# Kernel optimization log

Measured on AMD Instinct MI355X. Metric: run time of the kernel, lower is better.

## Reference

```python
import jax, jax.numpy as jnp
import numpy as np

E, C, M, H, O = 8, 1024, 2048, 8192, 2048  # experts, capacity, model_dim, hidden, output_dim


def setup_inputs() -> dict:
    key = jax.random.key(0)
    k1, k2, k3, k4, k5 = jax.random.split(key, 5)
    s1 = 1.0 / np.sqrt(M)
    s2 = 1.0 / np.sqrt(H)
    return {
        "x": jax.random.normal(k1, (E, C, M), dtype=jnp.float32),
        "fc1_w": jax.random.normal(k2, (E, H, M), dtype=jnp.float32) * s1,
        "fc1_b": jax.random.normal(k3, (E, H), dtype=jnp.float32) * s1,
        "fc2_w": jax.random.normal(k4, (E, H, O), dtype=jnp.float32) * s2,
        "fc2_b": jax.random.normal(k5, (E, O), dtype=jnp.float32) * s2,
    }


def reference(x, fc1_w, fc1_b, fc2_w, fc2_b):
    # grouped GEMM: per-expert FC1 + bias + ReLU + FC2 + bias
    # x: [E, C, M], fc1_w: [E, H, M], fc2_w: [E, H, O]
    y = jnp.einsum('ecm,ehm->ech', x, fc1_w) + fc1_b[:, None, :]   # [E, C, H]
    y = jax.nn.relu(y)
    y = jnp.einsum('ech,eho->eco', y, fc2_w) + fc2_b[:, None, :]   # [E, C, O]
    return y
```

## Files before the change

### kernel.cpp

```cpp
#include <hip/hip_runtime.h>
#include <hip/hip_bf16.h>
#include <stddef.h>

constexpr int E_ = 8;
constexpr int C_ = 1024;
constexpr int M_ = 2048;
constexpr int H_ = 8192;
constexpr int O_ = 2048;

typedef __bf16 bf16;
typedef __bf16 bf16x4 __attribute__((ext_vector_type(4)));
typedef __bf16 bf16x8 __attribute__((ext_vector_type(8)));
typedef float  f32x4  __attribute__((ext_vector_type(4)));

#define GLOAD16(src, dst)                                                        \
    __builtin_amdgcn_global_load_lds(                                            \
        (const __attribute__((address_space(1))) void*)(src),                    \
        (__attribute__((address_space(3))) void*)(dst), 16, 0, 0)

#define BARRIER()  __builtin_amdgcn_s_barrier()
#define LGKM0()    do { asm volatile("s_waitcnt lgkmcnt(0)" ::: "memory");       \
                        __builtin_amdgcn_sched_barrier(0); } while (0)
#define VMCNT(n)   asm volatile("s_waitcnt vmcnt(" #n ")" ::: "memory")

__global__ __launch_bounds__(256)
void cvt_f32_bf16(const float* __restrict__ in, bf16* __restrict__ out, size_t n)
{
    size_t i = ((size_t)blockIdx.x * blockDim.x + threadIdx.x) * 16;
    const size_t stride = (size_t)gridDim.x * blockDim.x * 16;
    for (; i < n; i += stride) {
        f32x4 v0 = *(const f32x4*)(in + i);
        f32x4 v1 = *(const f32x4*)(in + i + 4);
        f32x4 v2 = *(const f32x4*)(in + i + 8);
        f32x4 v3 = *(const f32x4*)(in + i + 12);
        bf16x8 o0, o1;
#pragma unroll
        for (int j = 0; j < 4; ++j) {
            o0[j] = (bf16)v0[j]; o0[j + 4] = (bf16)v1[j];
            o1[j] = (bf16)v2[j]; o1[j + 4] = (bf16)v3[j];
        }
        *(bf16x8*)(out + i)     = o0;
        *(bf16x8*)(out + i + 8) = o1;
    }
}

__global__ __launch_bounds__(256)
void transpose_w2(const float* __restrict__ W2, bf16* __restrict__ W2t, int e0)
{
    const int e  = e0 + blockIdx.z;
    const int oo = blockIdx.x;
    const int ho = blockIdx.y;
    const int tid = threadIdx.x;

    __shared__ bf16 t[64][72];

    const float* src = W2 + (size_t)e * H_ * O_ + (size_t)(ho * 64) * O_ + oo * 64;
#pragma unroll
    for (int p = 0; p < 4; ++p) {
        const int h  = p * 16 + (tid >> 4);
        const int o4 = (tid & 15) * 4;
        f32x4 v = *(const f32x4*)(src + (size_t)h * O_ + o4);
#pragma unroll
        for (int q = 0; q < 4; ++q) t[o4 + q][h] = (bf16)v[q];
    }
    __syncthreads();

    bf16* dst = W2t + (size_t)blockIdx.z * O_ * H_ + (size_t)(oo * 64) * H_ + ho * 64;
#pragma unroll
    for (int p2 = 0; p2 < 2; ++p2) {
        const int o  = p2 * 32 + (tid >> 3);
        const int h8 = (tid & 7) * 8;
        bf16x8 v = *(const bf16x8*)(&t[o][h8]);
        *(bf16x8*)(dst + (size_t)o * H_ + h8) = v;
    }
}

template<int KDIM, bool RELU_BF16>
__global__ __launch_bounds__(512, 2)
void gemm256(const bf16* __restrict__ A, const bf16* __restrict__ B,
             const float* __restrict__ bias, void* __restrict__ OutP,
             int nBM, int nBN)
{
    extern __shared__ char smem[];
    constexpr int K2  = KDIM * 2;
    constexpr int NIT = KDIM / 128;

    const int tid  = threadIdx.x;
    const int lane = tid & 63;
    const int wid  = tid >> 6;
    const int wr = wid >> 2, wc = wid & 3;
    const int fr = lane & 15, fq = lane >> 4;

    const int nwg = gridDim.x;
    const int cpx = nwg >> 3;
    const int b0  = blockIdx.x;
    const int wg  = (b0 & 7) * cpx + (b0 >> 3);
    const int per_e = nBM * nBN;
    const int e  = wg / per_e;
    const int rr = wg - e * per_e;
    const int bn = rr / nBM;
    const int bm = rr - bn * nBM;
    const int MROWS = nBM * 256;
    const int NROWS = nBN * 256;

    const char* Apan = (const char*)(A + (size_t)e * MROWS * KDIM + (size_t)bm * 256 * KDIM);
    const char* Bpan = (const char*)(B + (size_t)e * NROWS * KDIM + (size_t)bn * 256 * KDIM);

    const int r0  = tid >> 3;
    const int wsw = ((tid & 7) << 4) ^ ((r0 & 7) << 4);

    auto stageA = [&](int gk, int comp) {
        char* lds = smem + (gk & 1) * 65536 + comp * 16384 + tid * 16;
        const char* src = Apan + (size_t)((comp << 7) + r0) * K2 + (size_t)gk * 128 + wsw;
        GLOAD16(src, lds);
        GLOAD16(src + (size_t)64 * K2, lds + 8192);
    };
    auto stageB = [&](int gk, int comp2) {
        char* lds = smem + (gk & 1) * 65536 + 32768 + comp2 * 16384 + tid * 16;
        const char* src = Bpan + (size_t)((comp2 << 7) + r0) * K2 + (size_t)gk * 128 + wsw;
        GLOAD16(src, lds);
        GLOAD16(src + (size_t)64 * K2, lds + 8192);
    };

    const int frq = fr & 7;
    const int cA0 = ((fq    ) ^ frq) << 4;
    const int cA1 = ((4 | fq) ^ frq) << 4;
    const int aoff = wr * 16384 + fr * 128;
    const int boff = 32768 + (wc >> 1) * 16384 + (wc & 1) * 8192 + fr * 128;

    bf16x8 av[4][2];
    bf16x8 bv[4][2];
    f32x4 acc[8][4];
#pragma unroll
    for (int m = 0; m < 8; ++m)
#pragma unroll
        for (int n = 0; n < 4; ++n) acc[m][n] = (f32x4){0.f, 0.f, 0.f, 0.f};

    auto loadA = [&](const char* base, int mh) {
#pragma unroll
        for (int mm = 0; mm < 4; ++mm) {
            const char* p = base + aoff + (mh * 4 + mm) * 2048;
            av[mm][0] = *(const bf16x8*)(p + cA0);
            av[mm][1] = *(const bf16x8*)(p + cA1);
        }
    };
    auto loadB = [&](const char* base, int nh) {
#pragma unroll
        for (int nn = 0; nn < 2; ++nn) {
            const char* p = base + boff + (nh * 2 + nn) * 2048;
            bv[nh * 2 + nn][0] = *(const bf16x8*)(p + cA0);
            bv[nh * 2 + nn][1] = *(const bf16x8*)(p + cA1);
        }
    };
    auto mmaq = [&](int mh, int nh) {
        __builtin_amdgcn_s_setprio(1);
#pragma unroll
        for (int mm = 0; mm < 4; ++mm)
#pragma unroll
            for (int nn = 0; nn < 2; ++nn) {
                const int m = mh * 4 + mm, n = nh * 2 + nn;
                acc[m][n] = __builtin_amdgcn_mfma_f32_16x16x32_bf16(av[mm][0], bv[n][0], acc[m][n], 0, 0, 0);
                acc[m][n] = __builtin_amdgcn_mfma_f32_16x16x32_bf16(av[mm][1], bv[n][1], acc[m][n], 0, 0, 0);
            }
        __builtin_amdgcn_s_setprio(0);
    };

    stageB(0, 0); stageB(0, 1); stageA(0, 0); stageA(0, 1);
    stageB(1, 0); stageB(1, 1);
    VMCNT(4);
    BARRIER();

    for (int t = 0; t < NIT; ++t) {
        const bool nl = (t + 1 < NIT);
        const char* d0b = smem;
        const char* d1b = smem + 65536;
        const int ga = 2 * t + 1;
        const int gb = 2 * t + 2;
        const int gc = 2 * t + 3;

        loadB(d0b, 0); loadA(d0b, 0);
        stageA(ga, 0);
        BARRIER(); LGKM0();
        mmaq(0, 0);
        BARRIER();

        loadB(d0b, 1);
        stageA(ga, 1);
        BARRIER(); LGKM0();
        mmaq(0, 1);
        BARRIER();

        loadA(d0b, 1);
        if (nl) stageB(gb, 0);
        BARRIER(); LGKM0();
        mmaq(1, 1);
        BARRIER();

        if (nl) stageB(gb, 1);
        BARRIER(); LGKM0();
        mmaq(1, 0);
        if (nl) { VMCNT(4); } else { VMCNT(0); }
        BARRIER();

        loadB(d1b, 0); loadA(d1b, 0);
        if (nl) stageA(gb, 0);
        BARRIER(); LGKM0();
        mmaq(0, 0);
        BARRIER();

        loadB(d1b, 1);
        if (nl) stageA(gb, 1);
        BARRIER(); LGKM0();
        mmaq(0, 1);
        BARRIER();

        loadA(d1b, 1);
        if (nl) stageB(gc, 0);
        BARRIER(); LGKM0();
        mmaq(1, 1);
        BARRIER();

        if (nl) stageB(gc, 1);
        BARRIER(); LGKM0();
        mmaq(1, 0);
        if (nl) {
            VMCNT(4);
            BARRIER();
        }
    }

    const int gr0 = bm * 256 + wr * 128;
    const int gc0 = bn * 256 + wc * 64;
    if constexpr (RELU_BF16) {
        bf16* Out = (bf16*)OutP;
#pragma unroll
        for (int n = 0; n < 4; ++n) {
            const int col = gc0 + n * 16 + fr;
            const float bb = bias[(size_t)e * NROWS + col];
#pragma unroll
            for (int m = 0; m < 8; ++m)
#pragma unroll
                for (int j = 0; j < 4; ++j) {
                    float v = acc[m][n][j] + bb;
                    v = v > 0.f ? v : 0.f;
                    const int row = gr0 + m * 16 + fq * 4 + j;
                    Out[((size_t)e * MROWS + row) * NROWS + col] = (bf16)v;
                }
        }
    } else {
        float* Out = (float*)OutP;
#pragma unroll
        for (int n = 0; n < 4; ++n) {
            const int col = gc0 + n * 16 + fr;
            const float bb = bias[(size_t)e * NROWS + col];
#pragma unroll
            for (int m = 0; m < 8; ++m)
#pragma unroll
                for (int j = 0; j < 4; ++j) {
                    const int row = gr0 + m * 16 + fq * 4 + j;
                    Out[((size_t)e * MROWS + row) * NROWS + col] = acc[m][n][j] + bb;
                }
        }
    }
}

template<int KDIM, bool RELU_BF16>
__global__ __launch_bounds__(1024, 1)
void gemm256w16(const bf16* __restrict__ A, const bf16* __restrict__ B,
                const float* __restrict__ bias, void* __restrict__ OutP,
                int nBM, int nBN)
{
    extern __shared__ char smem[];
    constexpr int K2  = KDIM * 2;
    constexpr int NIT = KDIM / 128;

    const int tid  = threadIdx.x;
    const int lane = tid & 63;
    const int wid  = tid >> 6;
    const int wr = wid >> 2, wc = wid & 3;
    const int fr = lane & 15, fq = lane >> 4;

    const int nwg = gridDim.x;
    const int cpx = nwg >> 3;
    const int b0  = blockIdx.x;
    const int wg  = (b0 & 7) * cpx + (b0 >> 3);
    const int per_e = nBM * nBN;
    const int e  = wg / per_e;
    const int rr = wg - e * per_e;
    const int bn = rr / nBM;
    const int bm = rr - bn * nBM;
    const int MROWS = nBM * 256;
    const int NROWS = nBN * 256;

    const char* Apan = (const char*)(A + (size_t)e * MROWS * KDIM + (size_t)bm * 256 * KDIM);
    const char* Bpan = (const char*)(B + (size_t)e * NROWS * KDIM + (size_t)bn * 256 * KDIM);

    const int r0  = tid >> 3;
    const int wsw = ((tid & 7) << 4) ^ ((r0 & 7) << 4);

    auto stageA = [&](int gk, int comp) {
        char* lds = smem + (gk & 1) * 65536 + comp * 16384 + tid * 16;
        const char* src = Apan + (size_t)((comp << 7) + r0) * K2 + (size_t)gk * 128 + wsw;
        GLOAD16(src, lds);
    };
    auto stageB = [&](int gk, int comp2) {
        char* lds = smem + (gk & 1) * 65536 + 32768 + comp2 * 16384 + tid * 16;
        const char* src = Bpan + (size_t)((comp2 << 7) + r0) * K2 + (size_t)gk * 128 + wsw;
        GLOAD16(src, lds);
    };

    const int frq = fr & 7;
    const int cA0 = ((fq    ) ^ frq) << 4;
    const int cA1 = ((4 | fq) ^ frq) << 4;
    const int aoff = (wr >> 1) * 16384 + (wr & 1) * 8192 + fr * 128;
    const int boff = 32768 + (wc >> 1) * 16384 + (wc & 1) * 8192 + fr * 128;

    bf16x8 av[2][2];
    bf16x8 bv[4][2];
    f32x4 acc[4][4];
#pragma unroll
    for (int m = 0; m < 4; ++m)
#pragma unroll
        for (int n = 0; n < 4; ++n) acc[m][n] = (f32x4){0.f, 0.f, 0.f, 0.f};

    auto loadA = [&](const char* base, int mh) {
#pragma unroll
        for (int mm = 0; mm < 2; ++mm) {
            const char* p = base + aoff + (mh * 2 + mm) * 2048;
            av[mm][0] = *(const bf16x8*)(p + cA0);
            av[mm][1] = *(const bf16x8*)(p + cA1);
        }
    };
    auto loadB = [&](const char* base, int nh) {
#pragma unroll
        for (int nn = 0; nn < 2; ++nn) {
            const char* p = base + boff + (nh * 2 + nn) * 2048;
            bv[nh * 2 + nn][0] = *(const bf16x8*)(p + cA0);
            bv[nh * 2 + nn][1] = *(const bf16x8*)(p + cA1);
        }
    };
    auto mmaq = [&](int mh, int nh) {
        __builtin_amdgcn_s_setprio(1);
#pragma unroll
        for (int mm = 0; mm < 2; ++mm)
#pragma unroll
            for (int nn = 0; nn < 2; ++nn) {
                const int m = mh * 2 + mm, n = nh * 2 + nn;
                acc[m][n] = __builtin_amdgcn_mfma_f32_16x16x32_bf16(av[mm][0], bv[n][0], acc[m][n], 0, 0, 0);
                acc[m][n] = __builtin_amdgcn_mfma_f32_16x16x32_bf16(av[mm][1], bv[n][1], acc[m][n], 0, 0, 0);
            }
        __builtin_amdgcn_s_setprio(0);
    };

    stageB(0, 0); stageB(0, 1); stageA(0, 0); stageA(0, 1);
    stageB(1, 0); stageB(1, 1);
    VMCNT(2);
    BARRIER();

    for (int t = 0; t < NIT; ++t) {
        const bool nl = (t + 1 < NIT);
        const char* d0b = smem;
        const char* d1b = smem + 65536;
        const int ga = 2 * t + 1;
        const int gb = 2 * t + 2;
        const int gc = 2 * t + 3;

        loadB(d0b, 0); loadA(d0b, 0);
        stageA(ga, 0);
        BARRIER(); LGKM0();
        mmaq(0, 0);
        BARRIER();

        loadB(d0b, 1);
        stageA(ga, 1);
        BARRIER(); LGKM0();
        mmaq(0, 1);
        BARRIER();

        loadA(d0b, 1);
        if (nl) stageB(gb, 0);
        BARRIER(); LGKM0();
        mmaq(1, 1);
        BARRIER();

        if (nl) stageB(gb, 1);
        BARRIER(); LGKM0();
        mmaq(1, 0);
        if (nl) { VMCNT(2); } else { VMCNT(0); }
        BARRIER();

        loadB(d1b, 0); loadA(d1b, 0);
        if (nl) stageA(gb, 0);
        BARRIER(); LGKM0();
        mmaq(0, 0);
        BARRIER();

        loadB(d1b, 1);
        if (nl) stageA(gb, 1);
        BARRIER(); LGKM0();
        mmaq(0, 1);
        BARRIER();

        loadA(d1b, 1);
        if (nl) stageB(gc, 0);
        BARRIER(); LGKM0();
        mmaq(1, 1);
        BARRIER();

        if (nl) stageB(gc, 1);
        BARRIER(); LGKM0();
        mmaq(1, 0);
        if (nl) {
            VMCNT(2);
            BARRIER();
        }
    }

    const int gr0 = bm * 256 + wr * 64;
    const int gc0 = bn * 256 + wc * 64;
    if constexpr (RELU_BF16) {
        bf16* Out = (bf16*)OutP;
#pragma unroll
        for (int n = 0; n < 4; ++n) {
            const int col = gc0 + n * 16 + fr;
            const float bb = bias[(size_t)e * NROWS + col];
#pragma unroll
            for (int m = 0; m < 4; ++m)
#pragma unroll
                for (int j = 0; j < 4; ++j) {
                    float v = acc[m][n][j] + bb;
                    v = v > 0.f ? v : 0.f;
                    const int row = gr0 + m * 16 + fq * 4 + j;
                    Out[((size_t)e * MROWS + row) * NROWS + col] = (bf16)v;
                }
        }
    } else {
        float* Out = (float*)OutP;
#pragma unroll
        for (int n = 0; n < 4; ++n) {
            const int col = gc0 + n * 16 + fr;
            const float bb = bias[(size_t)e * NROWS + col];
#pragma unroll
            for (int m = 0; m < 4; ++m)
#pragma unroll
                for (int j = 0; j < 4; ++j) {
                    const int row = gr0 + m * 16 + fq * 4 + j;
                    Out[((size_t)e * MROWS + row) * NROWS + col] = acc[m][n][j] + bb;
                }
        }
    }
}

extern "C" void kernel_launch(void* const* d_in, const int* in_sizes, int n_in,
                              void* d_out, int out_size, void* d_ws, size_t ws_size,
                              hipStream_t stream)
{
    const float* x  = (const float*)d_in[0];
    const float* w1 = (const float*)d_in[1];
    const float* b1 = (const float*)d_in[2];
    const float* w2 = (const float*)d_in[3];
    const float* b2 = (const float*)d_in[4];
    float* out = (float*)d_out;

    (void)hipFuncSetAttribute(reinterpret_cast<const void*>(&gemm256w16<M_, true>),
                              hipFuncAttributeMaxDynamicSharedMemorySize, 131072);
    (void)hipFuncSetAttribute(reinterpret_cast<const void*>(&gemm256<H_, false>),
                              hipFuncAttributeMaxDynamicSharedMemorySize, 131072);

    const size_t xb_sz  = (size_t)E_ * C_ * M_ * sizeof(bf16);
    const size_t w1b_sz = (size_t)E_ * H_ * M_ * sizeof(bf16);
    const size_t w2t_sz = (size_t)E_ * O_ * H_ * sizeof(bf16);
    const size_t y1_sz  = (size_t)E_ * C_ * H_ * sizeof(bf16);

    if (ws_size >= xb_sz + w1b_sz + w2t_sz + y1_sz) {
        bf16* xb  = (bf16*)d_ws;
        bf16* w1b = (bf16*)((char*)d_ws + xb_sz);
        bf16* w2t = (bf16*)((char*)d_ws + xb_sz + w1b_sz);
        bf16* y1  = (bf16*)((char*)d_ws + xb_sz + w1b_sz + w2t_sz);

        cvt_f32_bf16<<<2048, 256, 0, stream>>>(x,  xb,  (size_t)E_ * C_ * M_);
        cvt_f32_bf16<<<2048, 256, 0, stream>>>(w1, w1b, (size_t)E_ * H_ * M_);
        transpose_w2<<<dim3(O_ / 64, H_ / 64, E_), 256, 0, stream>>>(w2, w2t, 0);

        gemm256w16<M_, true><<<dim3(8 * 4 * (H_ / 256)), 1024, 131072, stream>>>(
            xb, w1b, b1, y1, 4, H_ / 256);
        gemm256<H_, false><<<dim3(8 * 4 * (O_ / 256)), 512, 131072, stream>>>(
            y1, w2t, b2, out, 4, O_ / 256);
    } else {
        bf16* xb  = (bf16*)d_ws;
        bf16* w1b = (bf16*)((char*)d_ws + xb_sz / E_);
        bf16* w2t = (bf16*)((char*)d_ws + (xb_sz + w1b_sz) / E_);
        bf16* y1  = (bf16*)((char*)d_ws + (xb_sz + w1b_sz + w2t_sz) / E_);
        for (int e = 0; e < E_; ++e) {
            cvt_f32_bf16<<<512, 256, 0, stream>>>(x + (size_t)e * C_ * M_,  xb,  (size_t)C_ * M_);
            cvt_f32_bf16<<<2048, 256, 0, stream>>>(w1 + (size_t)e * H_ * M_, w1b, (size_t)H_ * M_);
            transpose_w2<<<dim3(O_ / 64, H_ / 64, 1), 256, 0, stream>>>(w2, w2t, e);
            gemm256w16<M_, true><<<dim3(4 * (H_ / 256)), 1024, 131072, stream>>>(
                xb, w1b, b1 + (size_t)e * H_, y1, 4, H_ / 256);
            gemm256<H_, false><<<dim3(4 * (O_ / 256)), 512, 131072, stream>>>(
                y1, w2t, b2 + (size_t)e * O_, out + (size_t)e * C_ * O_, 4, O_ / 256);
        }
    }
}
```

Measured before the change: 908.1 us.

## Fuse W2 fp32-to-bf16 transpose into FC2 GEMM B-tile staging

Removes the separate transpose_w2 kernel and its bf16 workspace. The FC2 GEMM now reads fp32 W2 directly through registers, converts it to bf16 and writes transposed, swizzled tiles into LDS inside the main loop. FC1 also moves from the 1024-thread 16-wave kernel back to the 512-thread gemm256 variant. This saves a full read and write pass over W2, but the in-loop B load becomes register-staged fp32 traffic with full vmcnt(0) waits instead of asynchronous direct-to-LDS loads, which may reduce overlap in the FC2 main loop.

```diff
diff --git a/kernel.cpp b/kernel.cpp
--- a/kernel.cpp
+++ b/kernel.cpp
@@ -44,37 +44,6 @@
     }
 }
 
-__global__ __launch_bounds__(256)
-void transpose_w2(const float* __restrict__ W2, bf16* __restrict__ W2t, int e0)
-{
-    const int e  = e0 + blockIdx.z;
-    const int oo = blockIdx.x;
-    const int ho = blockIdx.y;
-    const int tid = threadIdx.x;
-
-    __shared__ bf16 t[64][72];
-
-    const float* src = W2 + (size_t)e * H_ * O_ + (size_t)(ho * 64) * O_ + oo * 64;
-#pragma unroll
-    for (int p = 0; p < 4; ++p) {
-        const int h  = p * 16 + (tid >> 4);
-        const int o4 = (tid & 15) * 4;
-        f32x4 v = *(const f32x4*)(src + (size_t)h * O_ + o4);
-#pragma unroll
-        for (int q = 0; q < 4; ++q) t[o4 + q][h] = (bf16)v[q];
-    }
-    __syncthreads();
-
-    bf16* dst = W2t + (size_t)blockIdx.z * O_ * H_ + (size_t)(oo * 64) * H_ + ho * 64;
-#pragma unroll
-    for (int p2 = 0; p2 < 2; ++p2) {
-        const int o  = p2 * 32 + (tid >> 3);
-        const int h8 = (tid & 7) * 8;
-        bf16x8 v = *(const bf16x8*)(&t[o][h8]);
-        *(bf16x8*)(dst + (size_t)o * H_ + h8) = v;
-    }
-}
-
 template<int KDIM, bool RELU_BF16>
 __global__ __launch_bounds__(512, 2)
 void gemm256(const bf16* __restrict__ A, const bf16* __restrict__ B,
@@ -264,15 +233,15 @@
     }
 }
 
-template<int KDIM, bool RELU_BF16>
-__global__ __launch_bounds__(1024, 1)
-void gemm256w16(const bf16* __restrict__ A, const bf16* __restrict__ B,
-                const float* __restrict__ bias, void* __restrict__ OutP,
-                int nBM, int nBN)
+__global__ __launch_bounds__(512, 2)
+void gemm2tn(const bf16* __restrict__ A, const float* __restrict__ W2,
+             const float* __restrict__ bias, float* __restrict__ Out,
+             int nBM, int nBN)
 {
     extern __shared__ char smem[];
-    constexpr int K2  = KDIM * 2;
-    constexpr int NIT = KDIM / 128;
+    constexpr int KDIM = H_;
+    constexpr int K2   = KDIM * 2;
+    constexpr int NIT  = KDIM / 128;
 
     const int tid  = threadIdx.x;
     const int lane = tid & 63;
@@ -292,8 +261,9 @@
     const int MROWS = nBM * 256;
     const int NROWS = nBN * 256;
 
-    const char* Apan = (const char*)(A + (size_t)e * MROWS * KDIM + (size_t)bm * 256 * KDIM);
-    const char* Bpan = (const char*)(B + (size_t)e * NROWS * KDIM + (size_t)bn * 256 * KDIM);
+    const char*  Apan = (const char*)(A + (size_t)e * MROWS * KDIM + (size_t)bm * 256 * KDIM);
+    const float* W2e  = W2 + (size_t)e * (size_t)H_ * O_;
+    const int    bnCol = bn * 256;
 
     const int r0  = tid >> 3;
     const int wsw = ((tid & 7) << 4) ^ ((r0 & 7) << 4);
@@ -302,31 +272,49 @@
         char* lds = smem + (gk & 1) * 65536 + comp * 16384 + tid * 16;
         const char* src = Apan + (size_t)((comp << 7) + r0) * K2 + (size_t)gk * 128 + wsw;
         GLOAD16(src, lds);
-    };
-    auto stageB = [&](int gk, int comp2) {
-        char* lds = smem + (gk & 1) * 65536 + 32768 + comp2 * 16384 + tid * 16;
-        const char* src = Bpan + (size_t)((comp2 << 7) + r0) * K2 + (size_t)gk * 128 + wsw;
-        GLOAD16(src, lds);
+        GLOAD16(src + (size_t)64 * K2, lds + 8192);
+    };
+
+    const int o0 = (tid & 31) * 4;
+    const int h0 = (tid >> 5) * 4;
+    const int hsub = ((h0 & 4) << 1);
+    const int hchk = h0 >> 3;
+
+    auto loadB32T = [&](int g, int comp2, f32x4* d) {
+        const float* s = W2e + (size_t)(g * 64 + h0) * O_ + bnCol + comp2 * 128 + o0;
+#pragma unroll
+        for (int j = 0; j < 4; ++j) d[j] = *(const f32x4*)(s + (size_t)j * O_);
+    };
+    auto cvtwriteBT = [&](int g, int comp2, const f32x4* d) {
+        char* rg = smem + (g & 1) * 65536 + 32768 + comp2 * 16384;
+#pragma unroll
+        for (int c = 0; c < 4; ++c) {
+            bf16x4 w;
+            w[0] = (bf16)d[0][c]; w[1] = (bf16)d[1][c];
+            w[2] = (bf16)d[2][c]; w[3] = (bf16)d[3][c];
+            const int r = o0 + c;
+            *(bf16x4*)(rg + r * 128 + (((hchk ^ (r & 7)) << 4) | hsub)) = w;
+        }
     };
 
     const int frq = fr & 7;
     const int cA0 = ((fq    ) ^ frq) << 4;
     const int cA1 = ((4 | fq) ^ frq) << 4;
-    const int aoff = (wr >> 1) * 16384 + (wr & 1) * 8192 + fr * 128;
+    const int aoff = wr * 16384 + fr * 128;
     const int boff = 32768 + (wc >> 1) * 16384 + (wc & 1) * 8192 + fr * 128;
 
-    bf16x8 av[2][2];
+    bf16x8 av[4][2];
     bf16x8 bv[4][2];
-    f32x4 acc[4][4];
-#pragma unroll
-    for (int m = 0; m < 4; ++m)
+    f32x4 acc[8][4];
+#pragma unroll
+    for (int m = 0; m < 8; ++m)
 #pragma unroll
         for (int n = 0; n < 4; ++n) acc[m][n] = (f32x4){0.f, 0.f, 0.f, 0.f};
 
     auto loadA = [&](const char* base, int mh) {
 #pragma unroll
-        for (int mm = 0; mm < 2; ++mm) {
-            const char* p = base + aoff + (mh * 2 + mm) * 2048;
+        for (int mm = 0; mm < 4; ++mm) {
+            const char* p = base + aoff + (mh * 4 + mm) * 2048;
             av[mm][0] = *(const bf16x8*)(p + cA0);
             av[mm][1] = *(const bf16x8*)(p + cA1);
         }
@@ -342,20 +330,27 @@
     auto mmaq = [&](int mh, int nh) {
         __builtin_amdgcn_s_setprio(1);
 #pragma unroll
-        for (int mm = 0; mm < 2; ++mm)
+        for (int mm = 0; mm < 4; ++mm)
 #pragma unroll
             for (int nn = 0; nn < 2; ++nn) {
-                const int m = mh * 2 + mm, n = nh * 2 + nn;
+                const int m = mh * 4 + mm, n = nh * 2 + nn;
                 acc[m][n] = __builtin_amdgcn_mfma_f32_16x16x32_bf16(av[mm][0], bv[n][0], acc[m][n], 0, 0, 0);
                 acc[m][n] = __builtin_amdgcn_mfma_f32_16x16x32_bf16(av[mm][1], bv[n][1], acc[m][n], 0, 0, 0);
             }
         __builtin_amdgcn_s_setprio(0);
     };
 
-    stageB(0, 0); stageB(0, 1); stageA(0, 0); stageA(0, 1);
-    stageB(1, 0); stageB(1, 1);
-    VMCNT(2);
-    BARRIER();
+    {
+        f32x4 p0[4], p1[4];
+        loadB32T(0, 0, p0); loadB32T(0, 1, p1);
+        stageA(0, 0); stageA(0, 1);
+        cvtwriteBT(0, 0, p0); cvtwriteBT(0, 1, p1);
+        loadB32T(1, 0, p0); loadB32T(1, 1, p1);
+        cvtwriteBT(1, 0, p0); cvtwriteBT(1, 1, p1);
+        VMCNT(0);
+        asm volatile("s_waitcnt lgkmcnt(0)" ::: "memory");
+        BARRIER();
+    }
 
     for (int t = 0; t < NIT; ++t) {
         const bool nl = (t + 1 < NIT);
@@ -364,90 +359,74 @@
         const int ga = 2 * t + 1;
         const int gb = 2 * t + 2;
         const int gc = 2 * t + 3;
+        f32x4 d0[4], d1[4];
 
         loadB(d0b, 0); loadA(d0b, 0);
+        if (nl) loadB32T(gb, 0, d0);
         stageA(ga, 0);
         BARRIER(); LGKM0();
         mmaq(0, 0);
         BARRIER();
 
         loadB(d0b, 1);
+        if (nl) loadB32T(gb, 1, d1);
         stageA(ga, 1);
         BARRIER(); LGKM0();
         mmaq(0, 1);
         BARRIER();
 
         loadA(d0b, 1);
-        if (nl) stageB(gb, 0);
+        if (nl) cvtwriteBT(gb, 0, d0);
         BARRIER(); LGKM0();
         mmaq(1, 1);
         BARRIER();
 
-        if (nl) stageB(gb, 1);
+        if (nl) cvtwriteBT(gb, 1, d1);
         BARRIER(); LGKM0();
         mmaq(1, 0);
-        if (nl) { VMCNT(2); } else { VMCNT(0); }
+        VMCNT(0);
         BARRIER();
 
         loadB(d1b, 0); loadA(d1b, 0);
-        if (nl) stageA(gb, 0);
+        if (nl) { loadB32T(gc, 0, d0); stageA(gb, 0); }
         BARRIER(); LGKM0();
         mmaq(0, 0);
         BARRIER();
 
         loadB(d1b, 1);
-        if (nl) stageA(gb, 1);
+        if (nl) { loadB32T(gc, 1, d1); stageA(gb, 1); }
         BARRIER(); LGKM0();
         mmaq(0, 1);
         BARRIER();
 
         loadA(d1b, 1);
-        if (nl) stageB(gc, 0);
+        if (nl) cvtwriteBT(gc, 0, d0);
         BARRIER(); LGKM0();
         mmaq(1, 1);
         BARRIER();
 
-        if (nl) stageB(gc, 1);
+        if (nl) cvtwriteBT(gc, 1, d1);
         BARRIER(); LGKM0();
         mmaq(1, 0);
         if (nl) {
-            VMCNT(2);
+            VMCNT(0);
             BARRIER();
         }
     }
 
-    const int gr0 = bm * 256 + wr * 64;
+    const int gr0 = bm * 256 + wr * 128;
     const int gc0 = bn * 256 + wc * 64;
-    if constexpr (RELU_BF16) {
-        bf16* Out = (bf16*)OutP;
-#pragma unroll
-        for (int n = 0; n < 4; ++n) {
-            const int col = gc0 + n * 16 + fr;
-            const float bb = bias[(size_t)e * NROWS + col];
-#pragma unroll
-            for (int m = 0; m < 4; ++m)
-#pragma unroll
-                for (int j = 0; j < 4; ++j) {
-                    float v = acc[m][n][j] + bb;
-                    v = v > 0.f ? v : 0.f;
-                    const int row = gr0 + m * 16 + fq * 4 + j;
-                    Out[((size_t)e * MROWS + row) * NROWS + col] = (bf16)v;
-                }
-        }
-    } else {
-        float* Out = (float*)OutP;
-#pragma unroll
-        for (int n = 0; n < 4; ++n) {
-            const int col = gc0 + n * 16 + fr;
-            const float bb = bias[(size_t)e * NROWS + col];
-#pragma unroll
-            for (int m = 0; m < 4; ++m)
-#pragma unroll
-                for (int j = 0; j < 4; ++j) {
-                    const int row = gr0 + m * 16 + fq * 4 + j;
-                    Out[((size_t)e * MROWS + row) * NROWS + col] = acc[m][n][j] + bb;
-                }
-        }
+#pragma unroll
+    for (int n = 0; n < 4; ++n) {
+        const int col = gc0 + n * 16 + fr;
+        const float bb = bias[(size_t)e * NROWS + col];
+#pragma unroll
+        for (int m = 0; m < 8; ++m)
+#pragma unroll
+            for (int j = 0; j < 4; ++j) {
+                const int row = gr0 + m * 16 + fq * 4 + j;
+                Out[((size_t)e * MROWS + row) * NROWS + col] = acc[m][n][j] + bb;
+            }
     }
 }
 
@@ -462,43 +441,39 @@
     const float* b2 = (const float*)d_in[4];
     float* out = (float*)d_out;
 
-    (void)hipFuncSetAttribute(reinterpret_cast<const void*>(&gemm256w16<M_, true>),
+    (void)hipFuncSetAttribute(reinterpret_cast<const void*>(&gemm256<M_, true>),
                               hipFuncAttributeMaxDynamicSharedMemorySize, 131072);
-    (void)hipFuncSetAttribute(reinterpret_cast<const void*>(&gemm256<H_, false>),
+    (void)hipFuncSetAttribute(reinterpret_cast<const void*>(&gemm2tn),
                               hipFuncAttributeMaxDynamicSharedMemorySize, 131072);
 
     const size_t xb_sz  = (size_t)E_ * C_ * M_ * sizeof(bf16);
     const size_t w1b_sz = (size_t)E_ * H_ * M_ * sizeof(bf16);
-    const size_t w2t_sz = (size_t)E_ * O_ * H_ * sizeof(bf16);
     const size_t y1_sz  = (size_t)E_ * C_ * H_ * sizeof(bf16);
 
-    if (ws_size >= xb_sz + w1b_sz + w2t_sz + y1_sz) {
+    if (ws_size >= xb_sz + w1b_sz + y1_sz) {
         bf16* xb  = (bf16*)d_ws;
         bf16* w1b = (bf16*)((char*)d_ws + xb_sz);
-        bf16* w2t = (bf16*)((char*)d_ws + xb_sz + w1b_sz);
-        bf16* y1  = (bf16*)((char*)d_ws + xb_sz + w1b_sz + w2t_sz);
+        bf16* y1  = (bf16*)((char*)d_ws + xb_sz + w1b_sz);
 
         cvt_f32_bf16<<<2048, 256, 0, stream>>>(x,  xb,  (size_t)E_ * C_ * M_);
         cvt_f32_bf16<<<2048, 256, 0, stream>>>(w1, w1b, (size_t)E_ * H_ * M_);
-        transpose_w2<<<dim3(O_ / 64, H_ / 64, E_), 256, 0, stream>>>(w2, w2t, 0);
-
-        gemm256w16<M_, true><<<dim3(8 * 4 * (H_ / 256)), 1024, 131072, stream>>>(
+
+        gemm256<M_, true><<<dim3(8 * 4 * (H_ / 256)), 512, 131072, stream>>>(
             xb, w1b, b1, y1, 4, H_ / 256);
-        gemm256<H_, false><<<dim3(8 * 4 * (O_ / 256)), 512, 131072, stream>>>(
-            y1, w2t, b2, out, 4, O_ / 256);
+        gemm2tn<<<dim3(8 * 4 * (O_ / 256)), 512, 131072, stream>>>(
+            y1, w2, b2, out, 4, O_ / 256);
     } else {
         bf16* xb  = (bf16*)d_ws;
         bf16* w1b = (bf16*)((char*)d_ws + xb_sz / E_);
-        bf16* w2t = (bf16*)((char*)d_ws + (xb_sz + w1b_sz) / E_);
-        bf16* y1  = (bf16*)((char*)d_ws + (xb_sz + w1b_sz + w2t_sz) / E_);
+        bf16* y1  = (bf16*)((char*)d_ws + (xb_sz + w1b_sz) / E_);
         for (int e = 0; e < E_; ++e) {
             cvt_f32_bf16<<<512, 256, 0, stream>>>(x + (size_t)e * C_ * M_,  xb,  (size_t)C_ * M_);
             cvt_f32_bf16<<<2048, 256, 0, stream>>>(w1 + (size_t)e * H_ * M_, w1b, (size_t)H_ * M_);
-            transpose_w2<<<dim3(O_ / 64, H_ / 64, 1), 256, 0, stream>>>(w2, w2t, e);
-            gemm256w16<M_, true><<<dim3(4 * (H_ / 256)), 1024, 131072, stream>>>(
+            gemm256<M_, true><<<dim3(4 * (H_ / 256)), 512, 131072, stream>>>(
                 xb, w1b, b1 + (size_t)e * H_, y1, 4, H_ / 256);
-            gemm256<H_, false><<<dim3(4 * (O_ / 256)), 512, 131072, stream>>>(
-                y1, w2t, b2 + (size_t)e * O_, out + (size_t)e * C_ * O_, 4, O_ / 256);
+            gemm2tn<<<dim3(4 * (O_ / 256)), 512, 131072, stream>>>(
+                y1, w2 + (size_t)e * (size_t)H_ * O_, b2 + (size_t)e * O_,
+                out + (size_t)e * C_ * O_, 4, O_ / 256);
         }
     }
 }
```

New measurement: 913.5 us. Within noise of the previous version (+0.6%).

## Fuse fc1 weight fp32-to-bf16 conversion into the first GEMM's B-tile staging

Applied to the files above, without the earlier changes.

The separate conversion pass for fc1 weights is removed. The first GEMM now loads fp32 W1 tiles into registers, converts them to bf16 and writes them into swizzled LDS, and its block changes from 16 waves to 8 waves, each holding a 128x64 accumulator tile. This drops one full read/write pass over the 512 MB of fc1 weights and shrinks the workspace. In exchange, the GEMM reads twice as many bytes for B, uses more registers, and waits fully on vmcnt(0), which may weaken overlap. The transpose kernel's LDS padding and store path are also changed.

```diff
diff --git a/kernel.cpp b/kernel.cpp
--- a/kernel.cpp
+++ b/kernel.cpp
@@ -12,6 +12,7 @@
 typedef __bf16 bf16x4 __attribute__((ext_vector_type(4)));
 typedef __bf16 bf16x8 __attribute__((ext_vector_type(8)));
 typedef float  f32x4  __attribute__((ext_vector_type(4)));
+typedef unsigned uint4v __attribute__((ext_vector_type(4)));
 
 #define GLOAD16(src, dst)                                                        \
     __builtin_amdgcn_global_load_lds(                                            \
@@ -52,7 +53,7 @@
     const int ho = blockIdx.y;
     const int tid = threadIdx.x;
 
-    __shared__ bf16 t[64][72];
+    __shared__ bf16 t[64][66];
 
     const float* src = W2 + (size_t)e * H_ * O_ + (size_t)(ho * 64) * O_ + oo * 64;
 #pragma unroll
@@ -70,8 +71,9 @@
     for (int p2 = 0; p2 < 2; ++p2) {
         const int o  = p2 * 32 + (tid >> 3);
         const int h8 = (tid & 7) * 8;
-        bf16x8 v = *(const bf16x8*)(&t[o][h8]);
-        *(bf16x8*)(dst + (size_t)o * H_ + h8) = v;
+        const unsigned* s32 = (const unsigned*)&t[o][h8];
+        uint4v w; w[0] = s32[0]; w[1] = s32[1]; w[2] = s32[2]; w[3] = s32[3];
+        *(uint4v*)(dst + (size_t)o * H_ + h8) = w;
     }
 }
 
@@ -264,15 +266,15 @@
     }
 }
 
-template<int KDIM, bool RELU_BF16>
-__global__ __launch_bounds__(1024, 1)
-void gemm256w16(const bf16* __restrict__ A, const bf16* __restrict__ B,
-                const float* __restrict__ bias, void* __restrict__ OutP,
-                int nBM, int nBN)
+__global__ __launch_bounds__(512, 2)
+void gemm1f(const bf16* __restrict__ A, const float* __restrict__ W1,
+            const float* __restrict__ bias, bf16* __restrict__ Out,
+            int nBM, int nBN)
 {
     extern __shared__ char smem[];
-    constexpr int K2  = KDIM * 2;
-    constexpr int NIT = KDIM / 128;
+    constexpr int KDIM = M_;
+    constexpr int K2   = KDIM * 2;
+    constexpr int NIT  = KDIM / 128;
 
     const int tid  = threadIdx.x;
     const int lane = tid & 63;
@@ -292,8 +294,8 @@
     const int MROWS = nBM * 256;
     const int NROWS = nBN * 256;
 
-    const char* Apan = (const char*)(A + (size_t)e * MROWS * KDIM + (size_t)bm * 256 * KDIM);
-    const char* Bpan = (const char*)(B + (size_t)e * NROWS * KDIM + (size_t)bn * 256 * KDIM);
+    const char*  Apan   = (const char*)(A + (size_t)e * MROWS * KDIM + (size_t)bm * 256 * KDIM);
+    const float* Bpan32 = W1 + (size_t)e * NROWS * KDIM + (size_t)bn * 256 * KDIM;
 
     const int r0  = tid >> 3;
     const int wsw = ((tid & 7) << 4) ^ ((r0 & 7) << 4);
@@ -302,31 +304,54 @@
         char* lds = smem + (gk & 1) * 65536 + comp * 16384 + tid * 16;
         const char* src = Apan + (size_t)((comp << 7) + r0) * K2 + (size_t)gk * 128 + wsw;
         GLOAD16(src, lds);
-    };
-    auto stageB = [&](int gk, int comp2) {
-        char* lds = smem + (gk & 1) * 65536 + 32768 + comp2 * 16384 + tid * 16;
-        const char* src = Bpan + (size_t)((comp2 << 7) + r0) * K2 + (size_t)gk * 128 + wsw;
-        GLOAD16(src, lds);
+        GLOAD16(src + (size_t)64 * K2, lds + 8192);
+    };
+    auto loadB32 = [&](int g, f32x4* d) {
+        const float* s0 = Bpan32 + (size_t)r0 * KDIM + g * 64 + (tid & 7) * 8;
+        d[0] = *(const f32x4*)s0;
+        d[1] = *(const f32x4*)(s0 + 4);
+        d[2] = *(const f32x4*)(s0 + (size_t)64 * KDIM);
+        d[3] = *(const f32x4*)(s0 + (size_t)64 * KDIM + 4);
+        const float* s1 = s0 + (size_t)128 * KDIM;
+        d[4] = *(const f32x4*)s1;
+        d[5] = *(const f32x4*)(s1 + 4);
+        d[6] = *(const f32x4*)(s1 + (size_t)64 * KDIM);
+        d[7] = *(const f32x4*)(s1 + (size_t)64 * KDIM + 4);
+    };
+    auto cvtwriteB = [&](int g, const f32x4* d) {
+        bf16x8 h0, h1, h2, h3;
+#pragma unroll
+        for (int j = 0; j < 4; ++j) {
+            h0[j] = (bf16)d[0][j]; h0[4 + j] = (bf16)d[1][j];
+            h1[j] = (bf16)d[2][j]; h1[4 + j] = (bf16)d[3][j];
+            h2[j] = (bf16)d[4][j]; h2[4 + j] = (bf16)d[5][j];
+            h3[j] = (bf16)d[6][j]; h3[4 + j] = (bf16)d[7][j];
+        }
+        char* dst = smem + (g & 1) * 65536 + 32768 + r0 * 128 + wsw;
+        *(bf16x8*)dst = h0;
+        *(bf16x8*)(dst + 8192)  = h1;
+        *(bf16x8*)(dst + 16384) = h2;
+        *(bf16x8*)(dst + 24576) = h3;
     };
 
     const int frq = fr & 7;
     const int cA0 = ((fq    ) ^ frq) << 4;
     const int cA1 = ((4 | fq) ^ frq) << 4;
-    const int aoff = (wr >> 1) * 16384 + (wr & 1) * 8192 + fr * 128;
+    const int aoff = wr * 16384 + fr * 128;
     const int boff = 32768 + (wc >> 1) * 16384 + (wc & 1) * 8192 + fr * 128;
 
-    bf16x8 av[2][2];
+    bf16x8 av[4][2];
     bf16x8 bv[4][2];
-    f32x4 acc[4][4];
-#pragma unroll
-    for (int m = 0; m < 4; ++m)
+    f32x4 acc[8][4];
+#pragma unroll
+    for (int m = 0; m < 8; ++m)
 #pragma unroll
         for (int n = 0; n < 4; ++n) acc[m][n] = (f32x4){0.f, 0.f, 0.f, 0.f};
 
     auto loadA = [&](const char* base, int mh) {
 #pragma unroll
-        for (int mm = 0; mm < 2; ++mm) {
-            const char* p = base + aoff + (mh * 2 + mm) * 2048;
+        for (int mm = 0; mm < 4; ++mm) {
+            const char* p = base + aoff + (mh * 4 + mm) * 2048;
             av[mm][0] = *(const bf16x8*)(p + cA0);
             av[mm][1] = *(const bf16x8*)(p + cA1);
         }
@@ -342,19 +367,25 @@
     auto mmaq = [&](int mh, int nh) {
         __builtin_amdgcn_s_setprio(1);
 #pragma unroll
-        for (int mm = 0; mm < 2; ++mm)
+        for (int mm = 0; mm < 4; ++mm)
 #pragma unroll
             for (int nn = 0; nn < 2; ++nn) {
-                const int m = mh * 2 + mm, n = nh * 2 + nn;
+                const int m = mh * 4 + mm, n = nh * 2 + nn;
                 acc[m][n] = __builtin_amdgcn_mfma_f32_16x16x32_bf16(av[mm][0], bv[n][0], acc[m][n], 0, 0, 0);
                 acc[m][n] = __builtin_amdgcn_mfma_f32_16x16x32_bf16(av[mm][1], bv[n][1], acc[m][n], 0, 0, 0);
             }
         __builtin_amdgcn_s_setprio(0);
     };
 
-    stageB(0, 0); stageB(0, 1); stageA(0, 0); stageA(0, 1);
-    stageB(1, 0); stageB(1, 1);
-    VMCNT(2);
+    f32x4 pE[8], pO[8];
+
+    loadB32(0, pE); loadB32(1, pO);
+    stageA(0, 0); stageA(0, 1);
+    cvtwriteB(0, pE);
+    cvtwriteB(1, pO);
+    if (NIT > 1) loadB32(2, pE);
+    VMCNT(0);
+    asm volatile("s_waitcnt lgkmcnt(0)" ::: "memory");
     BARRIER();
 
     for (int t = 0; t < NIT; ++t) {
@@ -362,92 +393,71 @@
         const char* d0b = smem;
         const char* d1b = smem + 65536;
         const int ga = 2 * t + 1;
-        const int gb = 2 * t + 2;
-        const int gc = 2 * t + 3;
 
         loadB(d0b, 0); loadA(d0b, 0);
-        stageA(ga, 0);
+        if (nl) loadB32(2 * t + 3, pO);
+        stageA(ga, 0); stageA(ga, 1);
         BARRIER(); LGKM0();
         mmaq(0, 0);
         BARRIER();
 
         loadB(d0b, 1);
-        stageA(ga, 1);
         BARRIER(); LGKM0();
         mmaq(0, 1);
         BARRIER();
 
         loadA(d0b, 1);
-        if (nl) stageB(gb, 0);
+        if (nl) cvtwriteB(2 * t + 2, pE);
         BARRIER(); LGKM0();
         mmaq(1, 1);
         BARRIER();
 
-        if (nl) stageB(gb, 1);
         BARRIER(); LGKM0();
         mmaq(1, 0);
-        if (nl) { VMCNT(2); } else { VMCNT(0); }
+        VMCNT(0);
         BARRIER();
 
         loadB(d1b, 0); loadA(d1b, 0);
-        if (nl) stageA(gb, 0);
+        if (t + 2 < NIT) loadB32(2 * t + 4, pE);
+        if (nl) { stageA(2 * t + 2, 0); stageA(2 * t + 2, 1); }
         BARRIER(); LGKM0();
         mmaq(0, 0);
         BARRIER();
 
         loadB(d1b, 1);
-        if (nl) stageA(gb, 1);
         BARRIER(); LGKM0();
         mmaq(0, 1);
         BARRIER();
 
         loadA(d1b, 1);
-        if (nl) stageB(gc, 0);
+        if (nl) cvtwriteB(2 * t + 3, pO);
         BARRIER(); LGKM0();
         mmaq(1, 1);
         BARRIER();
 
-        if (nl) stageB(gc, 1);
         BARRIER(); LGKM0();
         mmaq(1, 0);
         if (nl) {
-            VMCNT(2);
+            VMCNT(0);
             BARRIER();
         }
     }
 
-    const int gr0 = bm * 256 + wr * 64;
+    const int gr0 = bm * 256 + wr * 128;
     const int gc0 = bn * 256 + wc * 64;
-    if constexpr (RELU_BF16) {
-        bf16* Out = (bf16*)OutP;
-#pragma unroll
-        for (int n = 0; n < 4; ++n) {
-            const int col = gc0 + n * 16 + fr;
-            const float bb = bias[(size_t)e * NROWS + col];
-#pragma unroll
-            for (int m = 0; m < 4; ++m)
-#pragma unroll
-                for (int j = 0; j < 4; ++j) {
-                    float v = acc[m][n][j] + bb;
-                    v = v > 0.f ? v : 0.f;
-                    const int row = gr0 + m * 16 + fq * 4 + j;
-                    Out[((size_t)e * MROWS + row) * NROWS + col] = (bf16)v;
-                }
-        }
-    } else {
-        float* Out = (float*)OutP;
-#pragma unroll
-        for (int n = 0; n < 4; ++n) {
-            const int col = gc0 + n * 16 + fr;
-            const float bb = bias[(size_t)e * NROWS + col];
-#pragma unroll
-            for (int m = 0; m < 4; ++m)
-#pragma unroll
-                for (int j = 0; j < 4; ++j) {
-                    const int row = gr0 + m * 16 + fq * 4 + j;
-                    Out[((size_t)e * MROWS + row) * NROWS + col] = acc[m][n][j] + bb;
-                }
-        }
+#pragma unroll
+    for (int n = 0; n < 4; ++n) {
+        const int col = gc0 + n * 16 + fr;
+        const float bb = bias[(size_t)e * NROWS + col];
+#pragma unroll
+        for (int m = 0; m < 8; ++m)
+#pragma unroll
+            for (int j = 0; j < 4; ++j) {
+                float v = acc[m][n][j] + bb;
+                v = v > 0.f ? v : 0.f;
+                const int row = gr0 + m * 16 + fq * 4 + j;
+                Out[((size_t)e * MROWS + row) * NROWS + col] = (bf16)v;
+            }
     }
 }
 
@@ -462,41 +472,37 @@
     const float* b2 = (const float*)d_in[4];
     float* out = (float*)d_out;
 
-    (void)hipFuncSetAttribute(reinterpret_cast<const void*>(&gemm256w16<M_, true>),
+    (void)hipFuncSetAttribute(reinterpret_cast<const void*>(&gemm1f),
                               hipFuncAttributeMaxDynamicSharedMemorySize, 131072);
     (void)hipFuncSetAttribute(reinterpret_cast<const void*>(&gemm256<H_, false>),
                               hipFuncAttributeMaxDynamicSharedMemorySize, 131072);
 
     const size_t xb_sz  = (size_t)E_ * C_ * M_ * sizeof(bf16);
-    const size_t w1b_sz = (size_t)E_ * H_ * M_ * sizeof(bf16);
     const size_t w2t_sz = (size_t)E_ * O_ * H_ * sizeof(bf16);
     const size_t y1_sz  = (size_t)E_ * C_ * H_ * sizeof(bf16);
 
-    if (ws_size >= xb_sz + w1b_sz + w2t_sz + y1_sz) {
+    if (ws_size >= xb_sz + w2t_sz + y1_sz) {
         bf16* xb  = (bf16*)d_ws;
-        bf16* w1b = (bf16*)((char*)d_ws + xb_sz);
-        bf16* w2t = (bf16*)((char*)d_ws + xb_sz + w1b_sz);
-        bf16* y1  = (bf16*)((char*)d_ws + xb_sz + w1b_sz + w2t_sz);
-
-        cvt_f32_bf16<<<2048, 256, 0, stream>>>(x,  xb,  (size_t)E_ * C_ * M_);
-        cvt_f32_bf16<<<2048, 256, 0, stream>>>(w1, w1b, (size_t)E_ * H_ * M_);
+        bf16* w2t = (bf16*)((char*)d_ws + xb_sz);
+        bf16* y1  = (bf16*)((char*)d_ws + xb_sz + w2t_sz);
+
+        cvt_f32_bf16<<<2048, 256, 0, stream>>>(x, xb, (size_t)E_ * C_ * M_);
         transpose_w2<<<dim3(O_ / 64, H_ / 64, E_), 256, 0, stream>>>(w2, w2t, 0);
 
-        gemm256w16<M_, true><<<dim3(8 * 4 * (H_ / 256)), 1024, 131072, stream>>>(
-            xb, w1b, b1, y1, 4, H_ / 256);
+        gemm1f<<<dim3(8 * 4 * (H_ / 256)), 512, 131072, stream>>>(
+            xb, w1, b1, y1, 4, H_ / 256);
         gemm256<H_, false><<<dim3(8 * 4 * (O_ / 256)), 512, 131072, stream>>>(
             y1, w2t, b2, out, 4, O_ / 256);
     } else {
         bf16* xb  = (bf16*)d_ws;
-        bf16* w1b = (bf16*)((char*)d_ws + xb_sz / E_);
-        bf16* w2t = (bf16*)((char*)d_ws + (xb_sz + w1b_sz) / E_);
-        bf16* y1  = (bf16*)((char*)d_ws + (xb_sz + w1b_sz + w2t_sz) / E_);
+        bf16* w2t = (bf16*)((char*)d_ws + (size_t)C_ * M_ * sizeof(bf16));
+        bf16* y1  = (bf16*)((char*)d_ws + (size_t)C_ * M_ * sizeof(bf16)
+                                        + (size_t)O_ * H_ * sizeof(bf16));
         for (int e = 0; e < E_; ++e) {
-            cvt_f32_bf16<<<512, 256, 0, stream>>>(x + (size_t)e * C_ * M_,  xb,  (size_t)C_ * M_);
-            cvt_f32_bf16<<<2048, 256, 0, stream>>>(w1 + (size_t)e * H_ * M_, w1b, (size_t)H_ * M_);
+            cvt_f32_bf16<<<512, 256, 0, stream>>>(x + (size_t)e * C_ * M_, xb, (size_t)C_ * M_);
             transpose_w2<<<dim3(O_ / 64, H_ / 64, 1), 256, 0, stream>>>(w2, w2t, e);
-            gemm256w16<M_, true><<<dim3(4 * (H_ / 256)), 1024, 131072, stream>>>(
-                xb, w1b, b1 + (size_t)e * H_, y1, 4, H_ / 256);
+            gemm1f<<<dim3(4 * (H_ / 256)), 512, 131072, stream>>>(
+                xb, w1 + (size_t)e * H_ * M_, b1 + (size_t)e * H_, y1, 4, H_ / 256);
             gemm256<H_, false><<<dim3(4 * (O_ / 256)), 512, 131072, stream>>>(
                 y1, w2t, b2 + (size_t)e * O_, out + (size_t)e * C_ * O_, 4, O_ / 256);
         }
```

Measured after the change: 1.363 ms. 50.1% more time.
